# Kernel optimization log

Measured on AMD Instinct MI355X. Metric: run time of the kernel, lower is better.

Reference implementation:

```python
import jax, jax.numpy as jnp
import numpy as np

N_NODES = 100000
N_EDGES = 3200000
F_IN = 512
F_OUT = 256


def setup_inputs() -> dict:
    key = jax.random.key(0)
    k1, k2, k3, k4, k5 = jax.random.split(key, 5)
    x = jax.random.normal(k1, (N_NODES, F_IN), dtype=jnp.float32)
    weights = jax.random.normal(k2, (F_IN, F_OUT), dtype=jnp.float32) * 0.05
    # sparse adjacency in COO, row-sorted (equivalent to the CSR torch.spmm uses)
    edge_row = jnp.sort(jax.random.randint(k3, (N_EDGES,), 0, N_NODES, dtype=jnp.int32))
    edge_col = jax.random.randint(k4, (N_EDGES,), 0, N_NODES, dtype=jnp.int32)
    edge_val = jax.random.uniform(k5, (N_EDGES,), dtype=jnp.float32)
    return {"x": x, "weights": weights, "edge_row": edge_row,
            "edge_col": edge_col, "edge_val": edge_val}


def reference(x, weights, edge_row, edge_col, edge_val):
    # support = input @ weights  (dense GEMM)
    support = jnp.matmul(x, weights)                      # [N, F_OUT]
    # output = spmm(adj, support): gather neighbor rows, scale, scatter-add
    gathered = support[edge_col] * edge_val[:, None]      # [E, F_OUT]
    out = jax.ops.segment_sum(gathered, edge_row, num_segments=N_NODES)
    return out
```

## Files before the change

kernel.cpp:

```cpp
#include <hip/hip_runtime.h>

#define N_NODES 100000
#define N_EDGES 3200000
#define F_IN 512
#define F_OUT 256

typedef short bf16x8 __attribute__((ext_vector_type(8)));
typedef short bf16x4 __attribute__((ext_vector_type(4)));
typedef float f32x4 __attribute__((ext_vector_type(4)));
typedef unsigned u32x4 __attribute__((ext_vector_type(4)));

__device__ __forceinline__ short f2b(float f) {
    unsigned u = __builtin_bit_cast(unsigned, f);
    u += 0x7fffu + ((u >> 16) & 1u);
    return (short)(u >> 16);
}
__device__ __forceinline__ float b2f(short s) {
    unsigned u = ((unsigned)(unsigned short)s) << 16;
    return __builtin_bit_cast(float, u);
}
__device__ __forceinline__ unsigned pack2(float f0, float f1) {
    unsigned u0 = __builtin_bit_cast(unsigned, f0) + 0x8000u;
    unsigned u1 = __builtin_bit_cast(unsigned, f1) + 0x8000u;
    return __builtin_amdgcn_perm(u1, u0, 0x07060302);
}
__device__ __forceinline__ void load_lds16(const float* g, void* l) {
    __builtin_amdgcn_global_load_lds(
        (const __attribute__((address_space(1))) unsigned*)g,
        (__attribute__((address_space(3))) unsigned*)l, 16, 0, 0);
}

__global__ void k_wconv(const float* __restrict__ W, short* __restrict__ Wt) {
    int idx = blockIdx.x * 256 + threadIdx.x;
    int k = idx >> 8;
    int n = idx & 255;
    Wt[n * F_IN + k] = f2b(W[idx]);
}

__global__ void k_rowptr(const int* __restrict__ erow, int* __restrict__ rp) {
    int i = blockIdx.x * 256 + threadIdx.x;
    if (i > N_NODES) return;
    int lo = 0, hi = N_EDGES;
    while (lo < hi) {
        int mid = (lo + hi) >> 1;
        if (erow[mid] < i) lo = mid + 1; else hi = mid;
    }
    rp[i] = lo;
}

__global__ __launch_bounds__(512, 4) void k_gemm(const float* __restrict__ X,
                                                 const short* __restrict__ Wt,
                                                 short* __restrict__ S) {
    __shared__ float As[128 * 32];
    const int tid  = threadIdx.x;
    const int wave = tid >> 6;
    const int lane = tid & 63;
    const int wr   = wave >> 2;
    const int wc   = wave & 3;
    const int l15  = lane & 15, quad = lane >> 4;
    const long row_base = (long)blockIdx.x * 128;

    f32x4 acc[4][4];
#pragma unroll
    for (int i = 0; i < 4; ++i)
#pragma unroll
        for (int j = 0; j < 4; ++j) acc[i][j] = (f32x4){0.f, 0.f, 0.f, 0.f};

    long gr0 = row_base + (tid >> 3);
    long gr1 = gr0 + 64;
    if (gr0 >= N_NODES) gr0 = N_NODES - 1;
    if (gr1 >= N_NODES) gr1 = N_NODES - 1;
    const float* gp0 = X + gr0 * F_IN + (tid & 7) * 4;
    const float* gp1 = X + gr1 * F_IN + (tid & 7) * 4;
    char* lds0 = (char*)As + wave * 1024;
    char* lds1 = (char*)As + 8192 + wave * 1024;

    const short* wtb = Wt + (wc * 64 + l15) * F_IN + quad * 8;
    const float* arow = As + (wr * 64 + l15) * 32 + quad * 8;

#pragma unroll 1
    for (int k0 = 0; k0 < F_IN; k0 += 32) {
        __syncthreads();
        load_lds16(gp0 + k0, lds0);
        load_lds16(gp1 + k0, lds1);
        __syncthreads();

        bf16x8 bfrag[4];
#pragma unroll
        for (int j = 0; j < 4; ++j)
            bfrag[j] = *(const bf16x8*)(wtb + j * 16 * F_IN + k0);

        bf16x8 afrag[4];
#pragma unroll
        for (int i = 0; i < 4; ++i) {
            const float* ap = arow + i * 16 * 32;
            f32x4 x0 = *(const f32x4*)ap;
            f32x4 x1 = *(const f32x4*)(ap + 4);
            u32x4 pv = { pack2(x0.x, x0.y), pack2(x0.z, x0.w),
                         pack2(x1.x, x1.y), pack2(x1.z, x1.w) };
            afrag[i] = __builtin_bit_cast(bf16x8, pv);
        }
#pragma unroll
        for (int i = 0; i < 4; ++i)
#pragma unroll
            for (int j = 0; j < 4; ++j)
                acc[i][j] = __builtin_amdgcn_mfma_f32_16x16x32_bf16(
                    afrag[i], bfrag[j], acc[i][j], 0, 0, 0);
    }

#pragma unroll
    for (int i = 0; i < 4; ++i) {
#pragma unroll
        for (int rg = 0; rg < 4; ++rg) {
            long gm = row_base + wr * 64 + i * 16 + quad * 4 + rg;
            if (gm < N_NODES) {
#pragma unroll
                for (int j = 0; j < 4; ++j) {
                    int gn = wc * 64 + j * 16 + l15;
                    S[gm * F_OUT + gn] = f2b(acc[i][j][rg]);
                }
            }
        }
    }
}

__global__ __launch_bounds__(256) void k_spmm(const short* __restrict__ S,
                                              const int* __restrict__ ecol,
                                              const float* __restrict__ ev,
                                              const int* __restrict__ rp,
                                              float* __restrict__ out) {
    const int wave = threadIdx.x >> 6, lane = threadIdx.x & 63;
    const int half = lane >> 5, hl = lane & 31;
    const int r = (blockIdx.x * 4 + wave) * 2 + half;
    const int lo = rp[r], hi = rp[r + 1];
    const short* sp = S + hl * 8;
    float a[8] = {0.f, 0.f, 0.f, 0.f, 0.f, 0.f, 0.f, 0.f};
    int e = lo;
    if (e < hi) {
        int c = ecol[e];
        float v = ev[e];
        bf16x8 s = *(const bf16x8*)(sp + (long)c * F_OUT);
        for (++e; e < hi; ++e) {
            int c2 = ecol[e];
            float v2 = ev[e];
            bf16x8 s2 = *(const bf16x8*)(sp + (long)c2 * F_OUT);
#pragma unroll
            for (int i = 0; i < 8; ++i) a[i] += v * b2f(s[i]);
            v = v2; s = s2;
        }
#pragma unroll
        for (int i = 0; i < 8; ++i) a[i] += v * b2f(s[i]);
    }
    f32x4 o0 = {a[0], a[1], a[2], a[3]};
    f32x4 o1 = {a[4], a[5], a[6], a[7]};
    float* op = out + (long)r * F_OUT + hl * 8;
    *(f32x4*)op = o0;
    *(f32x4*)(op + 4) = o1;
}

extern "C" void kernel_launch(void* const* d_in, const int* in_sizes, int n_in,
                              void* d_out, int out_size, void* d_ws, size_t ws_size,
                              hipStream_t stream) {
    const float* x    = (const float*)d_in[0];
    const float* w    = (const float*)d_in[1];
    const int*   erow = (const int*)d_in[2];
    const int*   ecol = (const int*)d_in[3];
    const float* ev   = (const float*)d_in[4];
    float* out = (float*)d_out;

    char* ws = (char*)d_ws;
    short* Wt = (short*)ws;
    int*   rp = (int*)(ws + 262144);
    short* S  = (short*)(ws + (1 << 20));

    k_wconv<<<512, 256, 0, stream>>>(w, Wt);
    k_rowptr<<<(N_NODES + 256) / 256, 256, 0, stream>>>(erow, rp);
    k_gemm<<<(N_NODES + 127) / 128, 512, 0, stream>>>(x, Wt, S);
    k_spmm<<<N_NODES / 8, 256, 0, stream>>>(S, ecol, ev, rp, out);
}
```

Baseline: 584.2 us.

## Software-pipeline GEMM A tiles via registers and batch SpMM gathers by four

The GEMM stops using direct global-to-LDS loads of fp32 X. It now prefetches X two k-steps ahead into registers, converts to bf16 once, and stores into a padded, double-buffered LDS tile, which leaves one barrier per k-step. The SpMM gather loop now keeps four neighbor rows in flight with clamped indices and zeroed weights for the tail, raising memory-level parallelism. The cost is higher register pressure and redundant clamped loads on short rows.

```diff
diff --git a/kernel.cpp b/kernel.cpp
--- a/kernel.cpp
+++ b/kernel.cpp
@@ -4,6 +4,8 @@
 #define N_EDGES 3200000
 #define F_IN 512
 #define F_OUT 256
+#define BK 32
+#define NK (F_IN / BK)
 
 typedef short bf16x8 __attribute__((ext_vector_type(8)));
 typedef short bf16x4 __attribute__((ext_vector_type(4)));
@@ -23,11 +25,6 @@
     unsigned u0 = __builtin_bit_cast(unsigned, f0) + 0x8000u;
     unsigned u1 = __builtin_bit_cast(unsigned, f1) + 0x8000u;
     return __builtin_amdgcn_perm(u1, u0, 0x07060302);
-}
-__device__ __forceinline__ void load_lds16(const float* g, void* l) {
-    __builtin_amdgcn_global_load_lds(
-        (const __attribute__((address_space(1))) unsigned*)g,
-        (__attribute__((address_space(3))) unsigned*)l, 16, 0, 0);
 }
 
 __global__ void k_wconv(const float* __restrict__ W, short* __restrict__ Wt) {
@@ -51,7 +48,7 @@
 __global__ __launch_bounds__(512, 4) void k_gemm(const float* __restrict__ X,
                                                  const short* __restrict__ Wt,
                                                  short* __restrict__ S) {
-    __shared__ float As[128 * 32];
+    __shared__ __align__(16) short As[2][128 * 40];
     const int tid  = threadIdx.x;
     const int wave = tid >> 6;
     const int lane = tid & 63;
@@ -66,46 +63,58 @@
 #pragma unroll
         for (int j = 0; j < 4; ++j) acc[i][j] = (f32x4){0.f, 0.f, 0.f, 0.f};
 
-    long gr0 = row_base + (tid >> 3);
-    long gr1 = gr0 + 64;
-    if (gr0 >= N_NODES) gr0 = N_NODES - 1;
-    if (gr1 >= N_NODES) gr1 = N_NODES - 1;
-    const float* gp0 = X + gr0 * F_IN + (tid & 7) * 4;
-    const float* gp1 = X + gr1 * F_IN + (tid & 7) * 4;
-    char* lds0 = (char*)As + wave * 1024;
-    char* lds1 = (char*)As + 8192 + wave * 1024;
+    const int srow = tid >> 2;
+    const int scol = (tid & 3) * 8;
+    long grow = row_base + srow;
+    if (grow >= N_NODES) grow = N_NODES - 1;
+    const float* gp = X + grow * F_IN + scol;
+    short* wp = &As[0][srow * 40 + scol];
 
     const short* wtb = Wt + (wc * 64 + l15) * F_IN + quad * 8;
-    const float* arow = As + (wr * 64 + l15) * 32 + quad * 8;
+    const short* arp = &As[0][(wr * 64 + l15) * 40 + quad * 8];
 
-#pragma unroll 1
-    for (int k0 = 0; k0 < F_IN; k0 += 32) {
-        __syncthreads();
-        load_lds16(gp0 + k0, lds0);
-        load_lds16(gp1 + k0, lds1);
-        __syncthreads();
+    f32x4 rlo[2], rhi[2];
+    rlo[0] = *(const f32x4*)(gp);
+    rhi[0] = *(const f32x4*)(gp + 4);
+    rlo[1] = *(const f32x4*)(gp + BK);
+    rhi[1] = *(const f32x4*)(gp + BK + 4);
+    {
+        u32x4 pv = { pack2(rlo[0].x, rlo[0].y), pack2(rlo[0].z, rlo[0].w),
+                     pack2(rhi[0].x, rhi[0].y), pack2(rhi[0].z, rhi[0].w) };
+        *(u32x4*)wp = pv;
+    }
 
+#pragma unroll
+    for (int k0 = 0; k0 < NK; ++k0) {
+        const int cur = k0 & 1;
+        if (k0 + 2 < NK) {
+            rlo[cur] = *(const f32x4*)(gp + (k0 + 2) * BK);
+            rhi[cur] = *(const f32x4*)(gp + (k0 + 2) * BK + 4);
+        }
         bf16x8 bfrag[4];
 #pragma unroll
         for (int j = 0; j < 4; ++j)
-            bfrag[j] = *(const bf16x8*)(wtb + j * 16 * F_IN + k0);
+            bfrag[j] = *(const bf16x8*)(wtb + j * 16 * F_IN + k0 * BK);
+
+        __syncthreads();
 
         bf16x8 afrag[4];
 #pragma unroll
-        for (int i = 0; i < 4; ++i) {
-            const float* ap = arow + i * 16 * 32;
-            f32x4 x0 = *(const f32x4*)ap;
-            f32x4 x1 = *(const f32x4*)(ap + 4);
-            u32x4 pv = { pack2(x0.x, x0.y), pack2(x0.z, x0.w),
-                         pack2(x1.x, x1.y), pack2(x1.z, x1.w) };
-            afrag[i] = __builtin_bit_cast(bf16x8, pv);
-        }
+        for (int i = 0; i < 4; ++i)
+            afrag[i] = *(const bf16x8*)(arp + cur * (128 * 40) + i * 16 * 40);
 #pragma unroll
         for (int i = 0; i < 4; ++i)
 #pragma unroll
             for (int j = 0; j < 4; ++j)
                 acc[i][j] = __builtin_amdgcn_mfma_f32_16x16x32_bf16(
                     afrag[i], bfrag[j], acc[i][j], 0, 0, 0);
+
+        if (k0 + 1 < NK) {
+            const int nxt = cur ^ 1;
+            u32x4 pv = { pack2(rlo[nxt].x, rlo[nxt].y), pack2(rlo[nxt].z, rlo[nxt].w),
+                         pack2(rhi[nxt].x, rhi[nxt].y), pack2(rhi[nxt].z, rhi[nxt].w) };
+            *(u32x4*)(wp + nxt * (128 * 40)) = pv;
+        }
     }
 
 #pragma unroll
@@ -135,21 +144,28 @@
     const int lo = rp[r], hi = rp[r + 1];
     const short* sp = S + hl * 8;
     float a[8] = {0.f, 0.f, 0.f, 0.f, 0.f, 0.f, 0.f, 0.f};
-    int e = lo;
-    if (e < hi) {
-        int c = ecol[e];
-        float v = ev[e];
-        bf16x8 s = *(const bf16x8*)(sp + (long)c * F_OUT);
-        for (++e; e < hi; ++e) {
-            int c2 = ecol[e];
-            float v2 = ev[e];
-            bf16x8 s2 = *(const bf16x8*)(sp + (long)c2 * F_OUT);
+    if (lo < hi) {
+        const int him1 = hi - 1;
+        float v[4]; bf16x8 s[4];
+#define FETCH(E, J) { int _e = (E); int _ee = _e < him1 ? _e : him1;            \
+                      float _vt = ev[_ee];                                      \
+                      v[J] = (_e < hi) ? _vt : 0.f;                             \
+                      s[J] = *(const bf16x8*)(sp + (long)ecol[_ee] * F_OUT); }
+        FETCH(lo + 0, 0); FETCH(lo + 1, 1); FETCH(lo + 2, 2); FETCH(lo + 3, 3);
+        for (int base = lo; base < hi; base += 4) {
+            float cv0 = v[0], cv1 = v[1], cv2 = v[2], cv3 = v[3];
+            bf16x8 cs0 = s[0], cs1 = s[1], cs2 = s[2], cs3 = s[3];
+            FETCH(base + 4, 0); FETCH(base + 5, 1);
+            FETCH(base + 6, 2); FETCH(base + 7, 3);
 #pragma unroll
-            for (int i = 0; i < 8; ++i) a[i] += v * b2f(s[i]);
-            v = v2; s = s2;
+            for (int i = 0; i < 8; ++i) {
+                a[i] += cv0 * b2f(cs0[i]);
+                a[i] += cv1 * b2f(cs1[i]);
+                a[i] += cv2 * b2f(cs2[i]);
+                a[i] += cv3 * b2f(cs3[i]);
+            }
         }
-#pragma unroll
-        for (int i = 0; i < 8; ++i) a[i] += v * b2f(s[i]);
+#undef FETCH
     }
     f32x4 o0 = {a[0], a[1], a[2], a[3]};
     f32x4 o1 = {a[4], a[5], a[6], a[7]};
```

Measured after the change: 602.9 us. 1.03x slower.
